# Kernel optimization log

Hardware: AMD Instinct MI355X
Metric: run time of the kernel (lower is better)

The kernel has to match this reference:

```python
import jax, jax.numpy as jnp
import numpy as np

NUM_HEADS = 16
HEAD_DIM = 64  # dim // num_heads


def setup_inputs() -> dict:
    key = jax.random.key(0)
    ks = jax.random.split(key, 4)
    B, N, C = 16, 4096, 1024
    s = 0.02
    x = jax.random.normal(ks[0], (B, N, C), dtype=jnp.float32)
    Wq = jax.random.normal(ks[1], (C, NUM_HEADS * HEAD_DIM), dtype=jnp.float32) * s
    Wkv = jax.random.normal(ks[2], (C, NUM_HEADS * HEAD_DIM * 2), dtype=jnp.float32) * s
    Wproj = jax.random.normal(ks[3], (NUM_HEADS * HEAD_DIM, C), dtype=jnp.float32) * s
    bproj = jnp.zeros((C,), dtype=jnp.float32)
    return {"x": x, "Wq": Wq, "Wkv": Wkv, "Wproj": Wproj, "bproj": bproj}


def reference(x, Wq, Wkv, Wproj, bproj):
    B, N, C = x.shape
    H, D = NUM_HEADS, HEAD_DIM
    scale = D ** (-0.5)
    # k, v projections over the full sequence: [B, N, 2, H, D]
    kv = (x @ Wkv).reshape(B, N, 2, H, D)
    k = kv[:, :, 0]  # [B, N, H, D]
    v = kv[:, :, 1]  # [B, N, H, D]
    # query from CLS token only: [B, 1, H, D]
    q = (x[:, :1, :] @ Wq).reshape(B, 1, H, D)
    # decode-style attention: single query attends over N keys
    attn = jnp.einsum("bqhd,bnhd->bhqn", q * scale, k)  # [B, H, 1, N]
    attn = jax.nn.softmax(attn, axis=-1)
    cls_embed = jnp.einsum("bhqn,bnhd->bqhd", attn, v).reshape(B, 1, H * D)
    return cls_embed @ Wproj + bproj  # [B, 1, C]
```

## Files before the change

### kernel.cpp

```cpp
#include <hip/hip_runtime.h>
#include <cstddef>
#include <cstdint>

#define B_ 16
#define N_ 4096
#define C_ 1024
#define H_ 16
#define D_ 64
#define HD_ 1024

__device__ __forceinline__ void stage16(const float* g, float* l, int lane) {
#if __has_builtin(__builtin_amdgcn_global_load_lds)
  __builtin_amdgcn_global_load_lds(
      (const __attribute__((address_space(1))) void*)g,
      (__attribute__((address_space(3))) void*)l, 16, 0, 0);
#else
  *(float4*)(l + lane * 4) = *(const float4*)g;
#endif
}

__global__ __launch_bounds__(256) void kA(const float* __restrict__ x,
                                          const float* __restrict__ Wq,
                                          const float* __restrict__ Wkv,
                                          float* __restrict__ u) {
  const int b = blockIdx.x >> 4;
  const int h = blockIdx.x & 15;
  __shared__ float xr[C_];
  __shared__ float qp[4][D_];
  __shared__ float qs[D_];
  const float* xb = x + (size_t)b * N_ * C_;
  for (int c = threadIdx.x; c < C_; c += 256) xr[c] = xb[c];
  __syncthreads();
  const int d = threadIdx.x & 63;
  const int part = threadIdx.x >> 6;
  float a = 0.f;
  const float* wq = Wq + h * D_ + d;
  #pragma unroll 4
  for (int c = part * 256; c < part * 256 + 256; ++c)
    a += xr[c] * wq[(size_t)c * HD_];
  qp[part][d] = a;
  __syncthreads();
  if (threadIdx.x < 64) {
    qs[threadIdx.x] = (qp[0][threadIdx.x] + qp[1][threadIdx.x] +
                       qp[2][threadIdx.x] + qp[3][threadIdx.x]) * 0.125f;
  }
  __syncthreads();
  for (int c = threadIdx.x; c < C_; c += 256) {
    const float4* wr = (const float4*)(Wkv + (size_t)c * (2 * HD_) + h * D_);
    float s = 0.f;
    #pragma unroll
    for (int d4 = 0; d4 < 16; ++d4) {
      float4 wv = wr[d4];
      s += wv.x * qs[4 * d4] + wv.y * qs[4 * d4 + 1] +
           wv.z * qs[4 * d4 + 2] + wv.w * qs[4 * d4 + 3];
    }
    u[(size_t)blockIdx.x * C_ + c] = s;
  }
}

__global__ __launch_bounds__(256, 2) void kF(const float* __restrict__ x,
                                             const float* __restrict__ u,
                                             float* __restrict__ wpart,
                                             float* __restrict__ mbuf,
                                             float* __restrict__ lbuf,
                                             int G) {
  const int b = blockIdx.y;
  const int chunk = blockIdx.x;
  const int CH = gridDim.x;
  const int tid = threadIdx.x;
  const int w = tid >> 6;
  const int lane = tid & 63;
  __shared__ float xs[2][8][C_];

  float4 uf[4][4];
  const float* ub = u + (size_t)(b * H_ + w * 4) * C_;
  #pragma unroll
  for (int hh = 0; hh < 4; ++hh)
    #pragma unroll
    for (int q = 0; q < 4; ++q)
      uf[hh][q] = *(const float4*)(ub + (size_t)hh * C_ + q * 256 + lane * 4);

  float4 acc[4][4];
  #pragma unroll
  for (int hh = 0; hh < 4; ++hh)
    #pragma unroll
    for (int q = 0; q < 4; ++q) acc[hh][q] = make_float4(0.f, 0.f, 0.f, 0.f);
  float m[4] = {-1e30f, -1e30f, -1e30f, -1e30f};
  float l[4] = {0.f, 0.f, 0.f, 0.f};

  const float* xb = x + ((size_t)b * N_ + (size_t)chunk * G * 8) * C_;

  #pragma unroll
  for (int r = 0; r < 8; ++r)
    stage16(xb + (size_t)r * C_ + w * 256 + lane * 4, &xs[0][r][w * 256], lane);

  for (int g = 0; g < G; ++g) {
    __syncthreads();
    if (g + 1 < G) {
      const float* xg = xb + (size_t)(g + 1) * 8 * C_;
      const int nb = (g + 1) & 1;
      #pragma unroll
      for (int r = 0; r < 8; ++r)
        stage16(xg + (size_t)r * C_ + w * 256 + lane * 4, &xs[nb][r][w * 256],
                lane);
    }
    const int buf = g & 1;
    #pragma unroll
    for (int r = 0; r < 8; ++r) {
      float4 xq[4];
      #pragma unroll
      for (int q = 0; q < 4; ++q)
        xq[q] = *(const float4*)&xs[buf][r][q * 256 + lane * 4];
      float ph[4];
      #pragma unroll
      for (int hh = 0; hh < 4; ++hh) {
        float a = 0.f;
        #pragma unroll
        for (int q = 0; q < 4; ++q)
          a += xq[q].x * uf[hh][q].x + xq[q].y * uf[hh][q].y +
               xq[q].z * uf[hh][q].z + xq[q].w * uf[hh][q].w;
        ph[hh] = a;
      }
      #pragma unroll
      for (int mask = 1; mask < 64; mask <<= 1) {
        #pragma unroll
        for (int hh = 0; hh < 4; ++hh) ph[hh] += __shfl_xor(ph[hh], mask);
      }
      float mn[4];
      #pragma unroll
      for (int hh = 0; hh < 4; ++hh) mn[hh] = fmaxf(m[hh], ph[hh]);
      if (mn[0] > m[0] || mn[1] > m[1] || mn[2] > m[2] || mn[3] > m[3]) {
        #pragma unroll
        for (int hh = 0; hh < 4; ++hh) {
          const float alpha = __expf(m[hh] - mn[hh]);
          l[hh] *= alpha;
          #pragma unroll
          for (int q = 0; q < 4; ++q) {
            acc[hh][q].x *= alpha; acc[hh][q].y *= alpha;
            acc[hh][q].z *= alpha; acc[hh][q].w *= alpha;
          }
          m[hh] = mn[hh];
        }
      }
      #pragma unroll
      for (int hh = 0; hh < 4; ++hh) {
        const float p = __expf(ph[hh] - m[hh]);
        l[hh] += p;
        #pragma unroll
        for (int q = 0; q < 4; ++q) {
          acc[hh][q].x += p * xq[q].x; acc[hh][q].y += p * xq[q].y;
          acc[hh][q].z += p * xq[q].z; acc[hh][q].w += p * xq[q].w;
        }
      }
    }
  }

  float* wp = wpart + ((size_t)(b * CH + chunk) * H_ + w * 4) * C_;
  #pragma unroll
  for (int hh = 0; hh < 4; ++hh)
    #pragma unroll
    for (int q = 0; q < 4; ++q)
      *(float4*)(wp + (size_t)hh * C_ + q * 256 + lane * 4) = acc[hh][q];
  if (lane == 0) {
    #pragma unroll
    for (int hh = 0; hh < 4; ++hh) {
      mbuf[(b * CH + chunk) * H_ + w * 4 + hh] = m[hh];
      lbuf[(b * CH + chunk) * H_ + w * 4 + hh] = l[hh];
    }
  }
}

__global__ __launch_bounds__(256) void kM(const float* __restrict__ wpart,
                                          const float* __restrict__ mbuf,
                                          const float* __restrict__ lbuf,
                                          float* __restrict__ w, int CH) {
  const int b = blockIdx.x >> 4;
  const int h = blockIdx.x & 15;
  const int t = threadIdx.x;
  __shared__ float alph[64];
  __shared__ float Linv;
  if (t < 64) {
    float mv = (t < CH) ? mbuf[(b * CH + t) * H_ + h] : -1e30f;
    float M = mv;
    #pragma unroll
    for (int mask = 1; mask < 64; mask <<= 1)
      M = fmaxf(M, __shfl_xor(M, mask));
    const float lv = (t < CH) ? lbuf[(b * CH + t) * H_ + h] : 0.f;
    const float a = __expf(mv - M);
    alph[t] = a;
    float L = a * lv;
    #pragma unroll
    for (int mask = 1; mask < 64; mask <<= 1) L += __shfl_xor(L, mask);
    if (t == 0) Linv = 1.f / L;
  }
  __syncthreads();
  float4 sum = make_float4(0.f, 0.f, 0.f, 0.f);
  for (int s = 0; s < CH; ++s) {
    const float a = alph[s];
    const float4 v =
        *(const float4*)(wpart + ((size_t)(b * CH + s) * H_ + h) * C_ + t * 4);
    sum.x += a * v.x; sum.y += a * v.y; sum.z += a * v.z; sum.w += a * v.w;
  }
  const float li = Linv;
  float4 o = make_float4(sum.x * li, sum.y * li, sum.z * li, sum.w * li);
  *(float4*)(w + (size_t)(b * H_ + h) * C_ + t * 4) = o;
}

__global__ __launch_bounds__(256) void kE1(const float* __restrict__ w,
                                           const float* __restrict__ Wkv,
                                           float* __restrict__ cls) {
  const int b = blockIdx.x >> 4;
  const int g = blockIdx.x & 15;
  const int t = threadIdx.x;
  const int j = t & 63;
  const int part = t >> 6;
  const float* wr = w + (size_t)(b * H_ + g) * C_ + part * 256;
  const float* wv = Wkv + 1024 + g * 64 + j;
  float acc = 0.f;
  #pragma unroll 8
  for (int c = 0; c < 256; ++c)
    acc += wr[c] * wv[(size_t)(part * 256 + c) * 2048];
  __shared__ float red[256];
  red[t] = acc;
  __syncthreads();
  if (t < 64) {
    const float s = red[t] + red[t + 64] + red[t + 128] + red[t + 192];
    cls[(size_t)b * HD_ + g * 64 + t] = s;
  }
}

__global__ __launch_bounds__(256) void kE2(const float* __restrict__ cls,
                                           const float* __restrict__ Wproj,
                                           const float* __restrict__ bproj,
                                           float* __restrict__ out) {
  const int b = blockIdx.x >> 4;
  const int g = blockIdx.x & 15;
  const int t = threadIdx.x;
  const int j = g * 64 + (t & 63);
  const int part = t >> 6;
  const float* cb = cls + (size_t)b * HD_ + part * 256;
  float acc = 0.f;
  #pragma unroll 8
  for (int i = 0; i < 256; ++i)
    acc += cb[i] * Wproj[(size_t)(part * 256 + i) * C_ + j];
  __shared__ float red[256];
  red[t] = acc;
  __syncthreads();
  if (t < 64) {
    const float s =
        red[t] + red[t + 64] + red[t + 128] + red[t + 192] + bproj[g * 64 + t];
    out[(size_t)b * C_ + g * 64 + t] = s;
  }
}

extern "C" void kernel_launch(void* const* d_in, const int* in_sizes, int n_in,
                              void* d_out, int out_size, void* d_ws,
                              size_t ws_size, hipStream_t stream) {
  const float* x = (const float*)d_in[0];
  const float* Wq = (const float*)d_in[1];
  const float* Wkv = (const float*)d_in[2];
  const float* Wproj = (const float*)d_in[3];
  const float* bproj = (const float*)d_in[4];
  float* ws = (float*)d_ws;

  int CH = 64;
  for (;;) {
    size_t fl = 262144ull + (size_t)CH * 262144ull + 2ull * CH * 256ull +
                262144ull + 16384ull;
    if (fl * 4ull <= ws_size || CH == 8) break;
    CH >>= 1;
  }
  const int G = N_ / (CH * 8);

  float* u = ws;
  float* wpart = u + 262144;
  float* mbuf = wpart + (size_t)CH * 262144ull;
  float* lbuf = mbuf + (size_t)CH * 256ull;
  float* w = lbuf + (size_t)CH * 256ull;
  float* cls = w + 262144;

  kA<<<dim3(B_ * H_), dim3(256), 0, stream>>>(x, Wq, Wkv, u);
  kF<<<dim3(CH, B_), dim3(256), 0, stream>>>(x, u, wpart, mbuf, lbuf, G);
  kM<<<dim3(256), dim3(256), 0, stream>>>(wpart, mbuf, lbuf, w, CH);
  kE1<<<dim3(256), dim3(256), 0, stream>>>(w, Wkv, cls);
  kE2<<<dim3(256), dim3(256), 0, stream>>>(cls, Wproj, bproj, (float*)d_out);
}
```

Measured before the change: 514.1 us.

## Split query/u precompute into two kernels and shrink kF staging for occupancy

Splits the combined q and u precompute into kA1 (q = x_cls·Wq, one block per 64-column slice and batch) and kA2 (u = Wk·q with coalesced reads plus wave shuffle reductions), adding a small q buffer to the workspace. Halves the rows staged per iteration in the main streaming kernel (8 to 4, double-buffered LDS 64KB to 32KB) and raises launch bounds to 4 blocks per CU for more latency hiding. Swaps block index mapping in the epilogue kernels so adjacent blocks share weight columns. Trades an extra launch and more loop iterations and barriers for better occupancy and coalescing.

```diff
diff --git a/kernel.cpp b/kernel.cpp
--- a/kernel.cpp
+++ b/kernel.cpp
@@ -19,46 +19,49 @@
 #endif
 }
 
-__global__ __launch_bounds__(256) void kA(const float* __restrict__ x,
-                                          const float* __restrict__ Wq,
-                                          const float* __restrict__ Wkv,
-                                          float* __restrict__ u) {
-  const int b = blockIdx.x >> 4;
-  const int h = blockIdx.x & 15;
-  __shared__ float xr[C_];
-  __shared__ float qp[4][D_];
-  __shared__ float qs[D_];
-  const float* xb = x + (size_t)b * N_ * C_;
-  for (int c = threadIdx.x; c < C_; c += 256) xr[c] = xb[c];
-  __syncthreads();
-  const int d = threadIdx.x & 63;
-  const int part = threadIdx.x >> 6;
-  float a = 0.f;
-  const float* wq = Wq + h * D_ + d;
+__global__ __launch_bounds__(256) void kA1(const float* __restrict__ x,
+                                           const float* __restrict__ Wq,
+                                           float* __restrict__ q) {
+  const int g = blockIdx.x >> 4;
+  const int b = blockIdx.x & 15;
+  const int t = threadIdx.x;
+  const int j = t & 63;
+  const int part = t >> 6;
+  const float* xr = x + (size_t)b * N_ * C_ + part * 256;
+  const float* wc = Wq + g * 64 + j;
+  float acc = 0.f;
+  #pragma unroll 8
+  for (int c = 0; c < 256; ++c)
+    acc += xr[c] * wc[(size_t)(part * 256 + c) * HD_];
+  __shared__ float red[256];
+  red[t] = acc;
+  __syncthreads();
+  if (t < 64) {
+    q[(size_t)b * HD_ + g * 64 + t] =
+        (red[t] + red[t + 64] + red[t + 128] + red[t + 192]) * 0.125f;
+  }
+}
+
+__global__ __launch_bounds__(256) void kA2(const float* __restrict__ q,
+                                           const float* __restrict__ Wkv,
+                                           float* __restrict__ u) {
+  const int h = blockIdx.x >> 4;
+  const int b = blockIdx.x & 15;
+  const int w = threadIdx.x >> 6;
+  const int j = threadIdx.x & 63;
+  const float qd = q[(size_t)b * HD_ + h * 64 + j];
+  const float* wk = Wkv + h * 64 + j;
+  float* ub = u + ((size_t)b * H_ + h) * C_;
   #pragma unroll 4
-  for (int c = part * 256; c < part * 256 + 256; ++c)
-    a += xr[c] * wq[(size_t)c * HD_];
-  qp[part][d] = a;
-  __syncthreads();
-  if (threadIdx.x < 64) {
-    qs[threadIdx.x] = (qp[0][threadIdx.x] + qp[1][threadIdx.x] +
-                       qp[2][threadIdx.x] + qp[3][threadIdx.x]) * 0.125f;
-  }
-  __syncthreads();
-  for (int c = threadIdx.x; c < C_; c += 256) {
-    const float4* wr = (const float4*)(Wkv + (size_t)c * (2 * HD_) + h * D_);
-    float s = 0.f;
-    #pragma unroll
-    for (int d4 = 0; d4 < 16; ++d4) {
-      float4 wv = wr[d4];
-      s += wv.x * qs[4 * d4] + wv.y * qs[4 * d4 + 1] +
-           wv.z * qs[4 * d4 + 2] + wv.w * qs[4 * d4 + 3];
-    }
-    u[(size_t)blockIdx.x * C_ + c] = s;
-  }
-}
-
-__global__ __launch_bounds__(256, 2) void kF(const float* __restrict__ x,
+  for (int c = w; c < C_; c += 4) {
+    float v = wk[(size_t)c * (2 * HD_)] * qd;
+    #pragma unroll
+    for (int mask = 1; mask < 64; mask <<= 1) v += __shfl_xor(v, mask);
+    if (j == 0) ub[c] = v;
+  }
+}
+
+__global__ __launch_bounds__(256, 4) void kF(const float* __restrict__ x,
                                              const float* __restrict__ u,
                                              float* __restrict__ wpart,
                                              float* __restrict__ mbuf,
@@ -70,7 +73,7 @@
   const int tid = threadIdx.x;
   const int w = tid >> 6;
   const int lane = tid & 63;
-  __shared__ float xs[2][8][C_];
+  __shared__ float xs[2][4][C_];
 
   float4 uf[4][4];
   const float* ub = u + (size_t)(b * H_ + w * 4) * C_;
@@ -88,25 +91,25 @@
   float m[4] = {-1e30f, -1e30f, -1e30f, -1e30f};
   float l[4] = {0.f, 0.f, 0.f, 0.f};
 
-  const float* xb = x + ((size_t)b * N_ + (size_t)chunk * G * 8) * C_;
-
-  #pragma unroll
-  for (int r = 0; r < 8; ++r)
+  const float* xb = x + ((size_t)b * N_ + (size_t)chunk * G * 4) * C_;
+
+  #pragma unroll
+  for (int r = 0; r < 4; ++r)
     stage16(xb + (size_t)r * C_ + w * 256 + lane * 4, &xs[0][r][w * 256], lane);
 
   for (int g = 0; g < G; ++g) {
     __syncthreads();
     if (g + 1 < G) {
-      const float* xg = xb + (size_t)(g + 1) * 8 * C_;
+      const float* xg = xb + (size_t)(g + 1) * 4 * C_;
       const int nb = (g + 1) & 1;
       #pragma unroll
-      for (int r = 0; r < 8; ++r)
+      for (int r = 0; r < 4; ++r)
         stage16(xg + (size_t)r * C_ + w * 256 + lane * 4, &xs[nb][r][w * 256],
                 lane);
     }
     const int buf = g & 1;
     #pragma unroll
-    for (int r = 0; r < 8; ++r) {
+    for (int r = 0; r < 4; ++r) {
       float4 xq[4];
       #pragma unroll
       for (int q = 0; q < 4; ++q)
@@ -209,8 +212,8 @@
 __global__ __launch_bounds__(256) void kE1(const float* __restrict__ w,
                                            const float* __restrict__ Wkv,
                                            float* __restrict__ cls) {
-  const int b = blockIdx.x >> 4;
-  const int g = blockIdx.x & 15;
+  const int g = blockIdx.x >> 4;
+  const int b = blockIdx.x & 15;
   const int t = threadIdx.x;
   const int j = t & 63;
   const int part = t >> 6;
@@ -233,8 +236,8 @@
                                            const float* __restrict__ Wproj,
                                            const float* __restrict__ bproj,
                                            float* __restrict__ out) {
-  const int b = blockIdx.x >> 4;
-  const int g = blockIdx.x & 15;
+  const int g = blockIdx.x >> 4;
+  const int b = blockIdx.x & 15;
   const int t = threadIdx.x;
   const int j = g * 64 + (t & 63);
   const int part = t >> 6;
@@ -265,21 +268,23 @@
 
   int CH = 64;
   for (;;) {
-    size_t fl = 262144ull + (size_t)CH * 262144ull + 2ull * CH * 256ull +
-                262144ull + 16384ull;
+    size_t fl = 16384ull + 262144ull + (size_t)CH * 262144ull +
+                2ull * CH * 256ull + 262144ull + 16384ull;
     if (fl * 4ull <= ws_size || CH == 8) break;
     CH >>= 1;
   }
-  const int G = N_ / (CH * 8);
-
-  float* u = ws;
+  const int G = N_ / (CH * 4);
+
+  float* q = ws;
+  float* u = q + 16384;
   float* wpart = u + 262144;
   float* mbuf = wpart + (size_t)CH * 262144ull;
   float* lbuf = mbuf + (size_t)CH * 256ull;
   float* w = lbuf + (size_t)CH * 256ull;
   float* cls = w + 262144;
 
-  kA<<<dim3(B_ * H_), dim3(256), 0, stream>>>(x, Wq, Wkv, u);
+  kA1<<<dim3(256), dim3(256), 0, stream>>>(x, Wq, q);
+  kA2<<<dim3(256), dim3(256), 0, stream>>>(q, Wkv, u);
   kF<<<dim3(CH, B_), dim3(256), 0, stream>>>(x, u, wpart, mbuf, lbuf, G);
   kM<<<dim3(256), dim3(256), 0, stream>>>(wpart, mbuf, lbuf, w, CH);
   kE1<<<dim3(256), dim3(256), 0, stream>>>(w, Wkv, cls);
```

Result: slower. 1.157 ms (+125.0%).
